# Kernel optimization log

Measured on AMD Instinct MI355X. Metric: run time of the kernel, lower is better.

## Reference

```python
import jax, jax.numpy as jnp
import numpy as np

B, L, D = 2, 2048, 2560
H, KV, HD = 8, 4, 256
FF = 10240
WINDOW = 1024
ROPE_BASE = 10000.0
EPS = 1e-6


def rmsnorm(x, scale=None):
    x32 = x.astype(jnp.float32)
    var = jnp.mean(jnp.square(x32), axis=-1, keepdims=True)
    xn = x32 * jax.lax.rsqrt(var + EPS)
    return xn if scale is None else xn * scale.astype(jnp.float32)


def apply_rope(x, positions, base):
    # full RoPE (rope_fraction=1.0): rotate pairs (i, i+head_dim//2)
    hd = x.shape[-1]
    half = hd // 2
    timescale = base ** (2.0 * jnp.arange(half, dtype=jnp.float32) / hd)
    ang = positions[:, :, None].astype(jnp.float32) / timescale  # [B,L,half]
    sin = jnp.sin(ang)[:, :, None, :]  # [B,L,1,half]
    cos = jnp.cos(ang)[:, :, None, :]
    x1, x2 = x[..., :half], x[..., half:]
    return jnp.concatenate([x1 * cos - x2 * sin, x2 * cos + x1 * sin], axis=-1)


def setup_inputs() -> dict:
    key = jax.random.key(0)
    ks = jax.random.split(key, 16)
    s = lambda fan_in: 1.0 / np.sqrt(fan_in)
    return {
        "x": jax.random.normal(ks[0], (B, L, D), jnp.float32),
        "positions": jnp.broadcast_to(jnp.arange(L, dtype=jnp.int32), (B, L)),
        "wq": jax.random.normal(ks[1], (D, H * HD), jnp.float32) * s(D),
        "wk": jax.random.normal(ks[2], (D, KV * HD), jnp.float32) * s(D),
        "wv": jax.random.normal(ks[3], (D, KV * HD), jnp.float32) * s(D),
        "wo": jax.random.normal(ks[4], (H * HD, D), jnp.float32) * s(H * HD),
        "q_scale": jnp.ones((HD,), jnp.float32),
        "k_scale": jnp.ones((HD,), jnp.float32),
        "pre_attn_scale": jnp.ones((D,), jnp.float32),
        "post_attn_scale": jnp.ones((D,), jnp.float32),
        "pre_ffw_scale": jnp.ones((D,), jnp.float32),
        "post_ffw_scale": jnp.ones((D,), jnp.float32),
        "w_gate": jax.random.normal(ks[5], (D, FF), jnp.float32) * s(D),
        "w_up": jax.random.normal(ks[6], (D, FF), jnp.float32) * s(D),
        "w_down": jax.random.normal(ks[7], (FF, D), jnp.float32) * s(FF),
    }


def reference(x, positions, wq, wk, wv, wo, q_scale, k_scale,
              pre_attn_scale, post_attn_scale, pre_ffw_scale, post_ffw_scale,
              w_gate, w_up, w_down):
    # --- attention sub-block ---
    h = rmsnorm(x, pre_attn_scale)
    q = (h @ wq).reshape(B, L, H, HD)
    k = (h @ wk).reshape(B, L, KV, HD)
    v = (h @ wv).reshape(B, L, KV, HD)
    q = apply_rope(rmsnorm(q, q_scale), positions, ROPE_BASE)
    k = apply_rope(rmsnorm(k, k_scale), positions, ROPE_BASE)
    v = rmsnorm(v)  # RMSNormNoScale on V
    rep = H // KV
    k = jnp.repeat(k, rep, axis=2)  # [B,L,H,HD]
    v = jnp.repeat(v, rep, axis=2)
    scores = jnp.einsum("bqhd,bkhd->bhqk", q, k)  # NOTE: no 1/sqrt(d) scaling, faithful to source
    i = jnp.arange(L)[:, None]
    j = jnp.arange(L)[None, :]
    mask = (j <= i) & (j > i - WINDOW)  # causal & sliding window
    scores = jnp.where(mask[None, None, :, :], scores, -10000.0)
    probs = jax.nn.softmax(scores.astype(jnp.float32), axis=-1)
    attn = jnp.einsum("bhqk,bkhd->bqhd", probs, v).reshape(B, L, H * HD)
    attn = attn @ wo
    x = x + rmsnorm(attn, post_attn_scale)
    # --- feedforward sub-block (GeGLU) ---
    h = rmsnorm(x, pre_ffw_scale)
    hidden = jax.nn.gelu(h @ w_gate, approximate=False) * (h @ w_up)
    ffw = hidden @ w_down
    x = x + rmsnorm(ffw, post_ffw_scale)
    return x
```

## Files before the change

### kernel.cpp

```cpp
#include <hip/hip_runtime.h>
#include <math.h>

#define DEV __device__ __forceinline__

typedef _Float16 f16;
typedef _Float16 f16x8 __attribute__((ext_vector_type(8)));
typedef _Float16 f16x4 __attribute__((ext_vector_type(4)));
typedef float f32x4 __attribute__((ext_vector_type(4)));

DEV void gload_lds16(const void* g, void* l) {
  __builtin_amdgcn_global_load_lds(
      (const __attribute__((address_space(1))) void*)g,
      (__attribute__((address_space(3))) void*)l, 16, 0, 0);
}

__global__ void transpose_w(const float* __restrict__ src, f16* __restrict__ dst,
                            int R, int C) {
  __shared__ float tile[32][33];
  int c0 = blockIdx.x * 32, r0 = blockIdx.y * 32;
  int tx = threadIdx.x, ty = threadIdx.y;
#pragma unroll
  for (int j = 0; j < 32; j += 8)
    tile[ty + j][tx] = src[(size_t)(r0 + ty + j) * C + c0 + tx];
  __syncthreads();
#pragma unroll
  for (int j = 0; j < 32; j += 8)
    dst[(size_t)(c0 + ty + j) * R + r0 + tx] = (f16)tile[tx][ty + j];
}

__global__ void rope_table_k(float* __restrict__ tab) {
  int idx = blockIdx.x * 256 + threadIdx.x;
  int pos = idx >> 7, j = idx & 127;
  float ts = powf(10000.0f, (float)j * (1.0f / 128.0f));
  float ang = (float)pos / ts;
  tab[pos * 256 + j] = sinf(ang);
  tab[pos * 256 + 128 + j] = cosf(ang);
}

__global__ __launch_bounds__(256) void rmsnorm_f32_f16(
    const float* __restrict__ in, const float* __restrict__ scale,
    f16* __restrict__ out) {
  constexpr int D = 2560, N4 = D / 4;
  const int m = blockIdx.x, tid = threadIdx.x;
  const float* row = in + (size_t)m * D;
  float vals[12];
  float ss = 0.f;
#pragma unroll
  for (int it = 0; it < 3; ++it) {
    int c4 = tid + it * 256;
    if (c4 < N4) {
      float4 v = *(const float4*)(row + c4 * 4);
      vals[it * 4 + 0] = v.x; vals[it * 4 + 1] = v.y;
      vals[it * 4 + 2] = v.z; vals[it * 4 + 3] = v.w;
      ss += v.x * v.x + v.y * v.y + v.z * v.z + v.w * v.w;
    }
  }
#pragma unroll
  for (int off = 32; off; off >>= 1) ss += __shfl_xor(ss, off, 64);
  __shared__ float red[4];
  if ((tid & 63) == 0) red[tid >> 6] = ss;
  __syncthreads();
  float rs = rsqrtf((red[0] + red[1] + red[2] + red[3]) * (1.0f / D) + 1e-6f);
#pragma unroll
  for (int it = 0; it < 3; ++it) {
    int c4 = tid + it * 256;
    if (c4 < N4) {
      float4 sc = *(const float4*)(scale + c4 * 4);
      f16x4 o;
      o[0] = (f16)(vals[it * 4 + 0] * rs * sc.x);
      o[1] = (f16)(vals[it * 4 + 1] * rs * sc.y);
      o[2] = (f16)(vals[it * 4 + 2] * rs * sc.z);
      o[3] = (f16)(vals[it * 4 + 3] * rs * sc.w);
      *(f16x4*)(out + (size_t)m * D + c4 * 4) = o;
    }
  }
}

__global__ __launch_bounds__(256) void residual_rmsnorm(
    const float* x, const f16* __restrict__ y,
    const float* __restrict__ scale, float* out) {
  constexpr int D = 2560, N4 = D / 4;
  const int m = blockIdx.x, tid = threadIdx.x;
  const f16* yr = y + (size_t)m * D;
  float yv[12];
  float ss = 0.f;
#pragma unroll
  for (int it = 0; it < 3; ++it) {
    int c4 = tid + it * 256;
    if (c4 < N4) {
      f16x4 u = *(const f16x4*)(yr + c4 * 4);
      float a = (float)u[0], b = (float)u[1], c = (float)u[2], d = (float)u[3];
      yv[it * 4 + 0] = a; yv[it * 4 + 1] = b; yv[it * 4 + 2] = c; yv[it * 4 + 3] = d;
      ss += a * a + b * b + c * c + d * d;
    }
  }
#pragma unroll
  for (int off = 32; off; off >>= 1) ss += __shfl_xor(ss, off, 64);
  __shared__ float red[4];
  if ((tid & 63) == 0) red[tid >> 6] = ss;
  __syncthreads();
  float rs = rsqrtf((red[0] + red[1] + red[2] + red[3]) * (1.0f / D) + 1e-6f);
#pragma unroll
  for (int it = 0; it < 3; ++it) {
    int c4 = tid + it * 256;
    if (c4 < N4) {
      float4 xv = *(const float4*)(x + (size_t)m * D + c4 * 4);
      float4 sc = *(const float4*)(scale + c4 * 4);
      float4 o;
      o.x = xv.x + yv[it * 4 + 0] * rs * sc.x;
      o.y = xv.y + yv[it * 4 + 1] * rs * sc.y;
      o.z = xv.z + yv[it * 4 + 2] * rs * sc.z;
      o.w = xv.w + yv[it * 4 + 3] * rs * sc.w;
      *(float4*)(out + (size_t)m * D + c4 * 4) = o;
    }
  }
}

__global__ __launch_bounds__(256) void norm_rope_k(
    const f16* __restrict__ qkv, const int* __restrict__ positions,
    const float* __restrict__ q_scale, const float* __restrict__ k_scale,
    const float* __restrict__ tab,
    f16* __restrict__ q_g, f16* __restrict__ k_g, f16* __restrict__ v_n) {
  const int m = blockIdx.x;
  const int tid = threadIdx.x, w = tid >> 6, l = tid & 63;
  const int pos = positions[m];
  const float* srow = tab + (size_t)pos * 256;
  const int c0 = l * 4;
  for (int vi = w; vi < 16; vi += 4) {
    f16x4 u = *(const f16x4*)(qkv + (size_t)m * 4096 + vi * 256 + c0);
    float x0 = (float)u[0], x1 = (float)u[1], x2 = (float)u[2], x3 = (float)u[3];
    float ss = x0 * x0 + x1 * x1 + x2 * x2 + x3 * x3;
#pragma unroll
    for (int off = 32; off; off >>= 1) ss += __shfl_xor(ss, off, 64);
    float rs = rsqrtf(ss * (1.0f / 256.0f) + 1e-6f);
    if (vi < 12) {
      const float* sc = (vi < 8) ? q_scale : k_scale;
      float4 s4 = *(const float4*)(sc + c0);
      float n0 = x0 * rs * s4.x, n1 = x1 * rs * s4.y;
      float n2 = x2 * rs * s4.z, n3 = x3 * rs * s4.w;
      float p0 = __shfl_xor(n0, 32, 64), p1 = __shfl_xor(n1, 32, 64);
      float p2 = __shfl_xor(n2, 32, 64), p3 = __shfl_xor(n3, 32, 64);
      int j0 = c0 & 127;
      float4 sn = *(const float4*)(srow + j0);
      float4 cs = *(const float4*)(srow + 128 + j0);
      float sgn = (l < 32) ? -1.0f : 1.0f;
      f16x4 o;
      o[0] = (f16)(n0 * cs.x + sgn * p0 * sn.x);
      o[1] = (f16)(n1 * cs.y + sgn * p1 * sn.y);
      o[2] = (f16)(n2 * cs.z + sgn * p2 * sn.z);
      o[3] = (f16)(n3 * cs.w + sgn * p3 * sn.w);
      if (vi < 8) *(f16x4*)(q_g + (size_t)m * 2048 + vi * 256 + c0) = o;
      else        *(f16x4*)(k_g + (size_t)m * 1024 + (vi - 8) * 256 + c0) = o;
    } else {
      f16x4 o;
      o[0] = (f16)(x0 * rs); o[1] = (f16)(x1 * rs);
      o[2] = (f16)(x2 * rs); o[3] = (f16)(x3 * rs);
      *(f16x4*)(v_n + (size_t)m * 1024 + (vi - 12) * 256 + c0) = o;
    }
  }
}

__global__ void transpose_v_k(const f16* __restrict__ v_n, f16* __restrict__ vt) {
  __shared__ f16 tile[32][33];
  int bkv = blockIdx.z;
  int b = bkv >> 2, kv = bkv & 3;
  int t0 = blockIdx.x * 32, d0 = blockIdx.y * 32;
  int tx = threadIdx.x, ty = threadIdx.y;
#pragma unroll
  for (int j = 0; j < 32; j += 8)
    tile[ty + j][tx] =
        v_n[(size_t)(b * 2048 + t0 + ty + j) * 1024 + kv * 256 + d0 + tx];
  __syncthreads();
#pragma unroll
  for (int j = 0; j < 32; j += 8)
    vt[((size_t)bkv * 256 + d0 + ty + j) * 2048 + t0 + tx] = tile[tx][ty + j];
}

template <int EPI>
__global__ __launch_bounds__(512, 2) void gemm256(
    const f16* __restrict__ A, const f16* __restrict__ BT,
    f16* __restrict__ C, const f16* __restrict__ aux, int M, int N, int K) {
  extern __shared__ __align__(16) f16 lds[];
  const int tid = threadIdx.x;
  const int w = tid >> 6, l = tid & 63;
  const int l15 = l & 15, lk = l >> 4;
  const int wm = w >> 2, wn = w & 3;

  const int orig = blockIdx.y * gridDim.x + blockIdx.x;
  const int bm = orig & 15;
  const int bn = orig >> 4;

  const int NT = K >> 6;

  const int srow = tid >> 2;
  const int sg = (tid & 3) ^ ((srow >> 1) & 3);
  const f16* pA1 = A + (size_t)(bm * 256 + srow) * K + sg * 8;
  const f16* pA2 = pA1 + (size_t)128 * K;
  const f16* pB1;
  const f16* pB2;
  if constexpr (EPI == 3) {
    pB1 = BT + (size_t)(bn * 128 + srow) * K + sg * 8;
    pB2 = aux + (size_t)(bn * 128 + srow) * K + sg * 8;
  } else {
    pB1 = BT + (size_t)(bn * 256 + srow) * K + sg * 8;
    pB2 = pB1 + (size_t)128 * K;
  }

  auto stage = [&](int op, int kh, int buf, int kt) {
    const int kb = kt * 64 + kh * 32;
    const f16* s1 = (op ? pB1 : pA1) + kb;
    const f16* s2 = (op ? pB2 : pA2) + kb;
    f16* dst = lds + ((buf << 2) + (kh << 1) + op) * 8192 + tid * 8;
    gload_lds16(s1, dst);
    gload_lds16(s2, dst + 4096);
  };

  const int fcol = (lk ^ ((l15 >> 1) & 3)) << 3;
  const int aoff = (wm * 128 + l15) * 32 + fcol;
  const int boff = 8192 + (wn * 64 + l15) * 32 + fcol;

  f32x4 acc[8][4] = {};

  stage(0, 0, 0, 0);
  stage(1, 0, 0, 0);
  stage(0, 1, 0, 0);
  stage(1, 1, 0, 0);
  if (NT > 1) stage(0, 0, 1, 1);
  asm volatile("s_waitcnt vmcnt(6)" ::: "memory");
  __builtin_amdgcn_s_barrier();
  asm volatile("" ::: "memory");

  for (int t = 0; t < NT; ++t) {
    const int buf = t & 1, nbuf = buf ^ 1;
    const f16* lb0 = lds + buf * 32768;
    const f16* lb1 = lb0 + 16384;
    {
      f16x8 a1[4], b[4], a2[4];
#pragma unroll
      for (int i = 0; i < 4; ++i) a1[i] = *(const f16x8*)(lb0 + aoff + i * 512);
#pragma unroll
      for (int i = 0; i < 4; ++i) b[i] = *(const f16x8*)(lb0 + boff + i * 512);
#pragma unroll
      for (int i = 0; i < 4; ++i) a2[i] = *(const f16x8*)(lb0 + aoff + (4 + i) * 512);
      if (t + 1 < NT) stage(1, 0, nbuf, t + 1);
      __builtin_amdgcn_s_setprio(1);
#pragma unroll
      for (int mi = 0; mi < 4; ++mi)
#pragma unroll
        for (int ni = 0; ni < 4; ++ni)
          acc[mi][ni] = __builtin_amdgcn_mfma_f32_16x16x32_f16(a1[mi], b[ni], acc[mi][ni], 0, 0, 0);
      __builtin_amdgcn_s_setprio(0);
      if (t + 1 < NT) stage(0, 1, nbuf, t + 1);
      __builtin_amdgcn_s_setprio(1);
#pragma unroll
      for (int mi = 0; mi < 4; ++mi)
#pragma unroll
        for (int ni = 0; ni < 4; ++ni)
          acc[4 + mi][ni] = __builtin_amdgcn_mfma_f32_16x16x32_f16(a2[mi], b[ni], acc[4 + mi][ni], 0, 0, 0);
      __builtin_amdgcn_s_setprio(0);
    }
    if (t + 1 < NT) asm volatile("s_waitcnt vmcnt(6)" ::: "memory");
    else            asm volatile("s_waitcnt vmcnt(0)" ::: "memory");
    __builtin_amdgcn_s_barrier();
    asm volatile("" ::: "memory");
    {
      f16x8 a1[4], b[4], a2[4];
#pragma unroll
      for (int i = 0; i < 4; ++i) a1[i] = *(const f16x8*)(lb1 + aoff + i * 512);
#pragma unroll
      for (int i = 0; i < 4; ++i) b[i] = *(const f16x8*)(lb1 + boff + i * 512);
#pragma unroll
      for (int i = 0; i < 4; ++i) a2[i] = *(const f16x8*)(lb1 + aoff + (4 + i) * 512);
      if (t + 1 < NT) stage(1, 1, nbuf, t + 1);
      __builtin_amdgcn_s_setprio(1);
#pragma unroll
      for (int mi = 0; mi < 4; ++mi)
#pragma unroll
        for (int ni = 0; ni < 4; ++ni)
          acc[mi][ni] = __builtin_amdgcn_mfma_f32_16x16x32_f16(a1[mi], b[ni], acc[mi][ni], 0, 0, 0);
      __builtin_amdgcn_s_setprio(0);
      if (t + 2 < NT) stage(0, 0, buf, t + 2);
      __builtin_amdgcn_s_setprio(1);
#pragma unroll
      for (int mi = 0; mi < 4; ++mi)
#pragma unroll
        for (int ni = 0; ni < 4; ++ni)
          acc[4 + mi][ni] = __builtin_amdgcn_mfma_f32_16x16x32_f16(a2[mi], b[ni], acc[4 + mi][ni], 0, 0, 0);
      __builtin_amdgcn_s_setprio(0);
    }
    if (t + 2 < NT)      asm volatile("s_waitcnt vmcnt(6)" ::: "memory");
    else if (t + 1 < NT) asm volatile("s_waitcnt vmcnt(4)" ::: "memory");
    else                 asm volatile("s_waitcnt vmcnt(0)" ::: "memory");
    __builtin_amdgcn_s_barrier();
    asm volatile("" ::: "memory");
  }

  if constexpr (EPI == 3) {
    constexpr int XP = 136;
    __syncthreads();
    f16* xls = lds;
    if (wn < 2) {
#pragma unroll
      for (int mi = 0; mi < 8; ++mi)
#pragma unroll
        for (int ni = 0; ni < 4; ++ni)
#pragma unroll
          for (int i = 0; i < 4; ++i) {
            int row = wm * 128 + mi * 16 + lk * 4 + i;
            int col = wn * 64 + ni * 16 + l15;
            float v = acc[mi][ni][i];
            v = 0.5f * v * (1.0f + erff(v * 0.70710678118654752f));
            xls[row * XP + col] = (f16)v;
          }
    }
    __syncthreads();
    if (wn >= 2) {
#pragma unroll
      for (int mi = 0; mi < 8; ++mi)
#pragma unroll
        for (int ni = 0; ni < 4; ++ni)
#pragma unroll
          for (int i = 0; i < 4; ++i) {
            int row = wm * 128 + mi * 16 + lk * 4 + i;
            int colg = (wn - 2) * 64 + ni * 16 + l15;
            float g = (float)xls[row * XP + colg];
            float v = g * acc[mi][ni][i];
            C[(size_t)(bm * 256 + row) * N + bn * 128 + colg] = (f16)v;
          }
    }
  } else {
#pragma unroll
    for (int mi = 0; mi < 8; ++mi) {
#pragma unroll
      for (int ni = 0; ni < 4; ++ni) {
#pragma unroll
        for (int i = 0; i < 4; ++i) {
          int row = bm * 256 + wm * 128 + mi * 16 + lk * 4 + i;
          int col = bn * 256 + wn * 64 + ni * 16 + l15;
          size_t idx = (size_t)row * N + col;
          float v = acc[mi][ni][i];
          if constexpr (EPI == 1) {
            v = 0.5f * v * (1.0f + erff(v * 0.70710678118654752f));
          } else if constexpr (EPI == 2) {
            v *= (float)aux[idx];
          }
          C[idx] = (f16)v;
        }
      }
    }
  }
}

__global__ __launch_bounds__(256) void flash_attn_k(
    const f16* __restrict__ q_g, const f16* __restrict__ k_g,
    const f16* __restrict__ vt, f16* __restrict__ ctx) {
  constexpr int KP = 264, VP = 40, PP = 40;
  __shared__ f16 Ks[32 * KP];
  __shared__ f16 Vs[256 * VP];
  __shared__ f16 Ps[4][16 * PP];
  const int qt = blockIdx.x, h = blockIdx.y, b = blockIdx.z;
  const int tid = threadIdx.x, w = tid >> 6, l = tid & 63;
  const int l15 = l & 15, lk = l >> 4;
  const int kv = h >> 1;

  f16x8 aq[8];
  const int qrow = qt * 64 + w * 16 + l15;
  const f16* qp = q_g + (size_t)(b * 2048 + qrow) * 2048 + h * 256 + lk * 8;
#pragma unroll
  for (int kc = 0; kc < 8; ++kc) aq[kc] = *(const f16x8*)(qp + kc * 32);

  f32x4 o[16] = {};
  float mrow[4] = {-1e30f, -1e30f, -1e30f, -1e30f};
  float lrow[4] = {0.f, 0.f, 0.f, 0.f};

  int kt_lo = 2 * qt - 32; if (kt_lo < 0) kt_lo = 0;
  const int kt_hi = 2 * qt + 1;
  const int iqb = qt * 64 + w * 16 + lk * 4;

  for (int kt = kt_lo; kt <= kt_hi; ++kt) {
    __syncthreads();
#pragma unroll
    for (int it = 0; it < 4; ++it) {
      int ch = tid + it * 256;
      int jl = ch >> 5, kcc = (ch & 31) * 8;
      *(f16x8*)&Ks[jl * KP + kcc] = *(const f16x8*)(
          k_g + (size_t)(b * 2048 + kt * 32 + jl) * 1024 + kv * 256 + kcc);
      int d = ch >> 2, tc = (ch & 3) * 8;
      *(f16x8*)&Vs[d * VP + tc] = *(const f16x8*)(
          vt + ((size_t)(b * 4 + kv) * 256 + d) * 2048 + kt * 32 + tc);
    }
    __syncthreads();
    f32x4 s[2] = {};
#pragma unroll
    for (int ct = 0; ct < 2; ++ct)
#pragma unroll
      for (int kc = 0; kc < 8; ++kc) {
        f16x8 bk = *(const f16x8*)&Ks[(ct * 16 + l15) * KP + kc * 32 + lk * 8];
        s[ct] = __builtin_amdgcn_mfma_f32_16x16x32_f16(aq[kc], bk, s[ct], 0, 0, 0);
      }
    float pm[4] = {-1e30f, -1e30f, -1e30f, -1e30f};
#pragma unroll
    for (int ct = 0; ct < 2; ++ct)
#pragma unroll
      for (int i = 0; i < 4; ++i) {
        int iq = iqb + i;
        int j = kt * 32 + ct * 16 + l15;
        bool valid = (j <= iq) && (j > iq - 1024);
        float sv = valid ? s[ct][i] : -1e30f;
        s[ct][i] = sv;
        pm[i] = fmaxf(pm[i], sv);
      }
#pragma unroll
    for (int i = 0; i < 4; ++i)
#pragma unroll
      for (int off = 1; off < 16; off <<= 1)
        pm[i] = fmaxf(pm[i], __shfl_xor(pm[i], off, 64));
    float corr[4], rsum[4];
#pragma unroll
    for (int i = 0; i < 4; ++i) {
      float mn = fmaxf(mrow[i], pm[i]);
      corr[i] = __expf(mrow[i] - mn);
      mrow[i] = mn;
      rsum[i] = 0.f;
    }
#pragma unroll
    for (int ct = 0; ct < 2; ++ct)
#pragma unroll
      for (int i = 0; i < 4; ++i) {
        float p = (s[ct][i] > -1e29f) ? __expf(s[ct][i] - mrow[i]) : 0.f;
        s[ct][i] = p;
        rsum[i] += p;
      }
#pragma unroll
    for (int i = 0; i < 4; ++i) {
#pragma unroll
      for (int off = 1; off < 16; off <<= 1) rsum[i] += __shfl_xor(rsum[i], off, 64);
      lrow[i] = lrow[i] * corr[i] + rsum[i];
    }
#pragma unroll
    for (int dt = 0; dt < 16; ++dt)
#pragma unroll
      for (int i = 0; i < 4; ++i) o[dt][i] *= corr[i];
#pragma unroll
    for (int ct = 0; ct < 2; ++ct)
#pragma unroll
      for (int i = 0; i < 4; ++i)
        Ps[w][(lk * 4 + i) * PP + ct * 16 + l15] = (f16)s[ct][i];
    __syncthreads();
    f16x8 pa = *(const f16x8*)&Ps[w][l15 * PP + lk * 8];
#pragma unroll
    for (int dt = 0; dt < 16; ++dt) {
      f16x8 bv = *(const f16x8*)&Vs[(dt * 16 + l15) * VP + lk * 8];
      o[dt] = __builtin_amdgcn_mfma_f32_16x16x32_f16(pa, bv, o[dt], 0, 0, 0);
    }
  }
  float inv[4];
#pragma unroll
  for (int i = 0; i < 4; ++i) inv[i] = 1.0f / lrow[i];
  f16* op = ctx + (size_t)(b * 2048 + qt * 64 + w * 16 + lk * 4) * 2048 + h * 256 + l15;
#pragma unroll
  for (int dt = 0; dt < 16; ++dt)
#pragma unroll
    for (int i = 0; i < 4; ++i)
      op[(size_t)i * 2048 + dt * 16] = (f16)(o[dt][i] * inv[i]);
}

extern "C" void kernel_launch(void* const* d_in, const int* in_sizes, int n_in,
                              void* d_out, int out_size, void* d_ws, size_t ws_size,
                              hipStream_t stream) {
  const float* x = (const float*)d_in[0];
  const int* positions = (const int*)d_in[1];
  const float* wq = (const float*)d_in[2];
  const float* wk = (const float*)d_in[3];
  const float* wv = (const float*)d_in[4];
  const float* wo = (const float*)d_in[5];
  const float* q_scale = (const float*)d_in[6];
  const float* k_scale = (const float*)d_in[7];
  const float* pre_attn = (const float*)d_in[8];
  const float* post_attn = (const float*)d_in[9];
  const float* pre_ffw = (const float*)d_in[10];
  const float* post_ffw = (const float*)d_in[11];
  const float* w_gate = (const float*)d_in[12];
  const float* w_up = (const float*)d_in[13];
  const float* w_down = (const float*)d_in[14];
  float* out = (float*)d_out;

  static bool s_attr = []() {
    hipFuncSetAttribute(reinterpret_cast<const void*>(&gemm256<0>),
                        hipFuncAttributeMaxDynamicSharedMemorySize, 131072);
    hipFuncSetAttribute(reinterpret_cast<const void*>(&gemm256<1>),
                        hipFuncAttributeMaxDynamicSharedMemorySize, 131072);
    hipFuncSetAttribute(reinterpret_cast<const void*>(&gemm256<2>),
                        hipFuncAttributeMaxDynamicSharedMemorySize, 131072);
    hipFuncSetAttribute(reinterpret_cast<const void*>(&gemm256<3>),
                        hipFuncAttributeMaxDynamicSharedMemorySize, 131072);
    return true;
  }();
  (void)s_attr;

  const size_t WT_BIG   = (size_t)20480 * 2560 * 2;
  const size_t WT_SMALL = (size_t)10240 * 2560 * 2;
  const size_t TAB_B = (size_t)2048 * 256 * 4;
  const size_t H_B   = (size_t)4096 * 2560 * 2;
  const size_t ACT_B = (size_t)92280832;
  auto aln = [](size_t v) { return (v + 255) & ~(size_t)255; };
  const bool big = ws_size >= aln(WT_BIG) + aln(TAB_B) + aln(H_B) + aln(ACT_B);

  char* ws = (char*)d_ws;
  size_t off = 0;
  auto alloc = [&](size_t bytes) {
    char* p = ws + off;
    off += (bytes + 255) & ~(size_t)255;
    return p;
  };
  f16* wT    = (f16*)alloc(big ? WT_BIG : WT_SMALL);
  float* tab = (float*)alloc(TAB_B);
  f16* h     = (f16*)alloc(H_B);
  char* act  = alloc(ACT_B);
  f16* qkv    = (f16*)(act);
  f16* q_g    = (f16*)(act + (size_t)33554432);
  f16* k_g    = (f16*)(act + (size_t)33554432 + 16777216);
  f16* v_n    = (f16*)(act + (size_t)33554432 + 16777216 + 8388608);
  f16* vtb    = (f16*)(act + (size_t)33554432 + 16777216 + 2 * 8388608);
  f16* ctx    = (f16*)(act + (size_t)33554432 + 16777216 + 3 * 8388608);
  f16* attn_o = (f16*)(act);
  f16* gbuf = (f16*)(act);
  f16* ffw  = h;
  f16* wuT  = wT + (size_t)10240 * 2560;
  (void)in_sizes; (void)n_in; (void)out_size;

  dim3 tb(32, 8);
  rope_table_k<<<1024, 256, 0, stream>>>(tab);

  rmsnorm_f32_f16<<<4096, 256, 0, stream>>>(x, pre_attn, h);
  transpose_w<<<dim3(2048 / 32, 2560 / 32), tb, 0, stream>>>(wq, wT, 2560, 2048);
  transpose_w<<<dim3(1024 / 32, 2560 / 32), tb, 0, stream>>>(wk, wT + (size_t)2048 * 2560, 2560, 1024);
  transpose_w<<<dim3(1024 / 32, 2560 / 32), tb, 0, stream>>>(wv, wT + (size_t)3072 * 2560, 2560, 1024);
  gemm256<0><<<dim3(4096 / 256, 4096 / 256), 512, 131072, stream>>>(h, wT, qkv, nullptr, 4096, 4096, 2560);
  norm_rope_k<<<4096, 256, 0, stream>>>(qkv, positions, q_scale, k_scale, tab, q_g, k_g, v_n);
  transpose_v_k<<<dim3(2048 / 32, 256 / 32, 8), tb, 0, stream>>>(v_n, vtb);
  flash_attn_k<<<dim3(32, 8, 2), 256, 0, stream>>>(q_g, k_g, vtb, ctx);
  transpose_w<<<dim3(2560 / 32, 2048 / 32), tb, 0, stream>>>(wo, wT, 2048, 2560);
  gemm256<0><<<dim3(2560 / 256, 4096 / 256), 512, 131072, stream>>>(ctx, wT, attn_o, nullptr, 4096, 2560, 2048);
  residual_rmsnorm<<<4096, 256, 0, stream>>>(x, attn_o, post_attn, out);

  rmsnorm_f32_f16<<<4096, 256, 0, stream>>>(out, pre_ffw, h);
  if (big) {
    transpose_w<<<dim3(10240 / 32, 2560 / 32), tb, 0, stream>>>(w_gate, wT, 2560, 10240);
    transpose_w<<<dim3(10240 / 32, 2560 / 32), tb, 0, stream>>>(w_up, wuT, 2560, 10240);
    gemm256<3><<<dim3(80, 16), 512, 131072, stream>>>(h, wT, gbuf, wuT, 4096, 10240, 2560);
  } else {
    transpose_w<<<dim3(10240 / 32, 2560 / 32), tb, 0, stream>>>(w_gate, wT, 2560, 10240);
    gemm256<1><<<dim3(10240 / 256, 4096 / 256), 512, 131072, stream>>>(h, wT, gbuf, nullptr, 4096, 10240, 2560);
    transpose_w<<<dim3(10240 / 32, 2560 / 32), tb, 0, stream>>>(w_up, wT, 2560, 10240);
    gemm256<2><<<dim3(10240 / 256, 4096 / 256), 512, 131072, stream>>>(h, wT, gbuf, gbuf, 4096, 10240, 2560);
  }
  transpose_w<<<dim3(2560 / 32, 10240 / 32), tb, 0, stream>>>(w_down, wT, 10240, 2560);
  gemm256<0><<<dim3(2560 / 256, 4096 / 256), 512, 131072, stream>>>(gbuf, wT, ffw, nullptr, 4096, 2560, 10240);
  residual_rmsnorm<<<4096, 256, 0, stream>>>(out, ffw, post_ffw, out);
}
```

Measured before the change: 1.196 ms.

## Add split-K for N=2560 GEMMs, vectorize weight transpose, fuse residual with pre-FFW norm

The output-projection and down-projection GEMMs (N=2560) launched only 160 tiles, so they now split K three ways into 480 blocks. The two extra partials are written as fp16 to workspace and summed inside the residual RMSNorm kernel. The weight transpose kernel moves to 64x64 tiles with float4 loads and 16-byte f16 stores. The post-attention residual is also fused with the pre-FFW RMSNorm, removing one kernel and one pass over the activations. In exchange, the partials add extra fp16 rounding and extra global traffic.

```diff
diff --git a/kernel.cpp b/kernel.cpp
--- a/kernel.cpp
+++ b/kernel.cpp
@@ -14,18 +14,31 @@
       (__attribute__((address_space(3))) void*)l, 16, 0, 0);
 }
 
-__global__ void transpose_w(const float* __restrict__ src, f16* __restrict__ dst,
-                            int R, int C) {
-  __shared__ float tile[32][33];
-  int c0 = blockIdx.x * 32, r0 = blockIdx.y * 32;
-  int tx = threadIdx.x, ty = threadIdx.y;
-#pragma unroll
-  for (int j = 0; j < 32; j += 8)
-    tile[ty + j][tx] = src[(size_t)(r0 + ty + j) * C + c0 + tx];
+__global__ __launch_bounds__(256) void transpose_w64(
+    const float* __restrict__ src, f16* __restrict__ dst, int R, int C) {
+  __shared__ float tile[64][65];
+  const int r0 = blockIdx.y * 64, c0 = blockIdx.x * 64;
+  const int tid = threadIdx.x;
+  const int rr = tid >> 4;
+  const int rc = (tid & 15) * 4;
+#pragma unroll
+  for (int p = 0; p < 4; ++p) {
+    int r = p * 16 + rr;
+    float4 v = *(const float4*)(src + (size_t)(r0 + r) * C + c0 + rc);
+    tile[r][rc] = v.x; tile[r][rc + 1] = v.y;
+    tile[r][rc + 2] = v.z; tile[r][rc + 3] = v.w;
+  }
   __syncthreads();
-#pragma unroll
-  for (int j = 0; j < 32; j += 8)
-    dst[(size_t)(c0 + ty + j) * R + r0 + tx] = (f16)tile[tx][ty + j];
+  const int wc = tid >> 3;
+  const int wk = (tid & 7) * 8;
+#pragma unroll
+  for (int p = 0; p < 2; ++p) {
+    int c = p * 32 + wc;
+    f16x8 o;
+#pragma unroll
+    for (int i = 0; i < 8; ++i) o[i] = (f16)tile[wk + i][c];
+    *(f16x8*)(dst + (size_t)(c0 + c) * R + r0 + wk) = o;
+  }
 }
 
 __global__ void rope_table_k(float* __restrict__ tab) {
@@ -76,42 +89,75 @@
   }
 }
 
-__global__ __launch_bounds__(256) void residual_rmsnorm(
-    const float* x, const f16* __restrict__ y,
-    const float* __restrict__ scale, float* out) {
+__global__ __launch_bounds__(256) void residual_rmsnorm3(
+    const float* __restrict__ x, const f16* __restrict__ y0,
+    const f16* __restrict__ y1, const f16* __restrict__ y2,
+    const float* __restrict__ scale, float* __restrict__ out,
+    const float* __restrict__ scale2, f16* __restrict__ h) {
   constexpr int D = 2560, N4 = D / 4;
   const int m = blockIdx.x, tid = threadIdx.x;
-  const f16* yr = y + (size_t)m * D;
+  const size_t base = (size_t)m * D;
+  __shared__ float red[4];
   float yv[12];
   float ss = 0.f;
 #pragma unroll
   for (int it = 0; it < 3; ++it) {
     int c4 = tid + it * 256;
     if (c4 < N4) {
-      f16x4 u = *(const f16x4*)(yr + c4 * 4);
+      f16x4 u = *(const f16x4*)(y0 + base + c4 * 4);
       float a = (float)u[0], b = (float)u[1], c = (float)u[2], d = (float)u[3];
+      if (y1) {
+        f16x4 v = *(const f16x4*)(y1 + base + c4 * 4);
+        f16x4 w2 = *(const f16x4*)(y2 + base + c4 * 4);
+        a += (float)v[0] + (float)w2[0]; b += (float)v[1] + (float)w2[1];
+        c += (float)v[2] + (float)w2[2]; d += (float)v[3] + (float)w2[3];
+      }
       yv[it * 4 + 0] = a; yv[it * 4 + 1] = b; yv[it * 4 + 2] = c; yv[it * 4 + 3] = d;
       ss += a * a + b * b + c * c + d * d;
     }
   }
 #pragma unroll
   for (int off = 32; off; off >>= 1) ss += __shfl_xor(ss, off, 64);
-  __shared__ float red[4];
   if ((tid & 63) == 0) red[tid >> 6] = ss;
   __syncthreads();
   float rs = rsqrtf((red[0] + red[1] + red[2] + red[3]) * (1.0f / D) + 1e-6f);
+  float ss2 = 0.f;
 #pragma unroll
   for (int it = 0; it < 3; ++it) {
     int c4 = tid + it * 256;
     if (c4 < N4) {
-      float4 xv = *(const float4*)(x + (size_t)m * D + c4 * 4);
+      float4 xv = *(const float4*)(x + base + c4 * 4);
       float4 sc = *(const float4*)(scale + c4 * 4);
       float4 o;
       o.x = xv.x + yv[it * 4 + 0] * rs * sc.x;
       o.y = xv.y + yv[it * 4 + 1] * rs * sc.y;
       o.z = xv.z + yv[it * 4 + 2] * rs * sc.z;
       o.w = xv.w + yv[it * 4 + 3] * rs * sc.w;
-      *(float4*)(out + (size_t)m * D + c4 * 4) = o;
+      *(float4*)(out + base + c4 * 4) = o;
+      yv[it * 4 + 0] = o.x; yv[it * 4 + 1] = o.y;
+      yv[it * 4 + 2] = o.z; yv[it * 4 + 3] = o.w;
+      ss2 += o.x * o.x + o.y * o.y + o.z * o.z + o.w * o.w;
+    }
+  }
+  if (h) {
+#pragma unroll
+    for (int off = 32; off; off >>= 1) ss2 += __shfl_xor(ss2, off, 64);
+    __syncthreads();
+    if ((tid & 63) == 0) red[tid >> 6] = ss2;
+    __syncthreads();
+    float rs2 = rsqrtf((red[0] + red[1] + red[2] + red[3]) * (1.0f / D) + 1e-6f);
+#pragma unroll
+    for (int it = 0; it < 3; ++it) {
+      int c4 = tid + it * 256;
+      if (c4 < N4) {
+        float4 sc = *(const float4*)(scale2 + c4 * 4);
+        f16x4 o;
+        o[0] = (f16)(yv[it * 4 + 0] * rs2 * sc.x);
+        o[1] = (f16)(yv[it * 4 + 1] * rs2 * sc.y);
+        o[2] = (f16)(yv[it * 4 + 2] * rs2 * sc.z);
+        o[3] = (f16)(yv[it * 4 + 3] * rs2 * sc.w);
+        *(f16x4*)(h + base + c4 * 4) = o;
+      }
     }
   }
 }
@@ -179,7 +225,8 @@
 template <int EPI>
 __global__ __launch_bounds__(512, 2) void gemm256(
     const f16* __restrict__ A, const f16* __restrict__ BT,
-    f16* __restrict__ C, const f16* __restrict__ aux, int M, int N, int K) {
+    f16* __restrict__ C, f16* __restrict__ aux, int M, int N, int K,
+    int kt0, int ktn) {
   extern __shared__ __align__(16) f16 lds[];
   const int tid = threadIdx.x;
   const int w = tid >> 6, l = tid & 63;
@@ -188,21 +235,35 @@
 
   const int orig = blockIdx.y * gridDim.x + blockIdx.x;
   const int bm = orig & 15;
-  const int bn = orig >> 4;
-
-  const int NT = K >> 6;
+  int bn, sK = 0;
+  if constexpr (EPI == 4) {
+    const int nper = (((int)(gridDim.x * gridDim.y)) >> 4) / 3;
+    const int q = orig >> 4;
+    bn = q % nper; sK = q / nper;
+  } else {
+    bn = orig >> 4;
+  }
+  int kt0v, ktnv;
+  if constexpr (EPI == 4) {
+    const int qt = ktn / 3, r = ktn % 3;
+    ktnv = qt + (sK < r ? 1 : 0);
+    kt0v = sK * qt + (sK < r ? sK : r);
+  } else {
+    kt0v = kt0; ktnv = ktn;
+  }
+  const int NT = ktnv;
 
   const int srow = tid >> 2;
   const int sg = (tid & 3) ^ ((srow >> 1) & 3);
-  const f16* pA1 = A + (size_t)(bm * 256 + srow) * K + sg * 8;
+  const f16* pA1 = A + (size_t)(bm * 256 + srow) * K + sg * 8 + kt0v * 64;
   const f16* pA2 = pA1 + (size_t)128 * K;
   const f16* pB1;
   const f16* pB2;
   if constexpr (EPI == 3) {
-    pB1 = BT + (size_t)(bn * 128 + srow) * K + sg * 8;
-    pB2 = aux + (size_t)(bn * 128 + srow) * K + sg * 8;
+    pB1 = BT + (size_t)(bn * 128 + srow) * K + sg * 8 + kt0v * 64;
+    pB2 = aux + (size_t)(bn * 128 + srow) * K + sg * 8 + kt0v * 64;
   } else {
-    pB1 = BT + (size_t)(bn * 256 + srow) * K + sg * 8;
+    pB1 = BT + (size_t)(bn * 256 + srow) * K + sg * 8 + kt0v * 64;
     pB2 = pB1 + (size_t)128 * K;
   }
 
@@ -329,6 +390,10 @@
           }
     }
   } else {
+    f16* Co = C;
+    if constexpr (EPI == 4) {
+      if (sK) Co = aux + (size_t)(sK - 1) * ((size_t)M * N);
+    }
 #pragma unroll
     for (int mi = 0; mi < 8; ++mi) {
 #pragma unroll
@@ -344,7 +409,7 @@
           } else if constexpr (EPI == 2) {
             v *= (float)aux[idx];
           }
-          C[idx] = (f16)v;
+          Co[idx] = (f16)v;
         }
       }
     }
@@ -493,6 +558,8 @@
     hipFuncSetAttribute(reinterpret_cast<const void*>(&gemm256<2>),
                         hipFuncAttributeMaxDynamicSharedMemorySize, 131072);
     hipFuncSetAttribute(reinterpret_cast<const void*>(&gemm256<3>),
+                        hipFuncAttributeMaxDynamicSharedMemorySize, 131072);
+    hipFuncSetAttribute(reinterpret_cast<const void*>(&gemm256<4>),
                         hipFuncAttributeMaxDynamicSharedMemorySize, 131072);
     return true;
   }();
@@ -527,35 +594,47 @@
   f16* gbuf = (f16*)(act);
   f16* ffw  = h;
   f16* wuT  = wT + (size_t)10240 * 2560;
+  f16* ap1  = wuT;
+  f16* fp1  = wT;
   (void)in_sizes; (void)n_in; (void)out_size;
 
-  dim3 tb(32, 8);
   rope_table_k<<<1024, 256, 0, stream>>>(tab);
 
   rmsnorm_f32_f16<<<4096, 256, 0, stream>>>(x, pre_attn, h);
-  transpose_w<<<dim3(2048 / 32, 2560 / 32), tb, 0, stream>>>(wq, wT, 2560, 2048);
-  transpose_w<<<dim3(1024 / 32, 2560 / 32), tb, 0, stream>>>(wk, wT + (size_t)2048 * 2560, 2560, 1024);
-  transpose_w<<<dim3(1024 / 32, 2560 / 32), tb, 0, stream>>>(wv, wT + (size_t)3072 * 2560, 2560, 1024);
-  gemm256<0><<<dim3(4096 / 256, 4096 / 256), 512, 131072, stream>>>(h, wT, qkv, nullptr, 4096, 4096, 2560);
+  transpose_w64<<<dim3(2048 / 64, 2560 / 64), 256, 0, stream>>>(wq, wT, 2560, 2048);
+  transpose_w64<<<dim3(1024 / 64, 2560 / 64), 256, 0, stream>>>(wk, wT + (size_t)2048 * 2560, 2560, 1024);
+  transpose_w64<<<dim3(1024 / 64, 2560 / 64), 256, 0, stream>>>(wv, wT + (size_t)3072 * 2560, 2560, 1024);
+  gemm256<0><<<dim3(16, 16), 512, 131072, stream>>>(h, wT, qkv, nullptr, 4096, 4096, 2560, 0, 40);
   norm_rope_k<<<4096, 256, 0, stream>>>(qkv, positions, q_scale, k_scale, tab, q_g, k_g, v_n);
-  transpose_v_k<<<dim3(2048 / 32, 256 / 32, 8), tb, 0, stream>>>(v_n, vtb);
+  transpose_v_k<<<dim3(2048 / 32, 256 / 32, 8), dim3(32, 8), 0, stream>>>(v_n, vtb);
   flash_attn_k<<<dim3(32, 8, 2), 256, 0, stream>>>(q_g, k_g, vtb, ctx);
-  transpose_w<<<dim3(2560 / 32, 2048 / 32), tb, 0, stream>>>(wo, wT, 2048, 2560);
-  gemm256<0><<<dim3(2560 / 256, 4096 / 256), 512, 131072, stream>>>(ctx, wT, attn_o, nullptr, 4096, 2560, 2048);
-  residual_rmsnorm<<<4096, 256, 0, stream>>>(x, attn_o, post_attn, out);
-
-  rmsnorm_f32_f16<<<4096, 256, 0, stream>>>(out, pre_ffw, h);
+  transpose_w64<<<dim3(2560 / 64, 2048 / 64), 256, 0, stream>>>(wo, wT, 2048, 2560);
   if (big) {
-    transpose_w<<<dim3(10240 / 32, 2560 / 32), tb, 0, stream>>>(w_gate, wT, 2560, 10240);
-    transpose_w<<<dim3(10240 / 32, 2560 / 32), tb, 0, stream>>>(w_up, wuT, 2560, 10240);
-    gemm256<3><<<dim3(80, 16), 512, 131072, stream>>>(h, wT, gbuf, wuT, 4096, 10240, 2560);
+    gemm256<4><<<dim3(30, 16), 512, 131072, stream>>>(ctx, wT, attn_o, ap1, 4096, 2560, 2048, 0, 32);
+    residual_rmsnorm3<<<4096, 256, 0, stream>>>(x, attn_o, ap1, ap1 + (size_t)4096 * 2560,
+                                                post_attn, out, pre_ffw, h);
   } else {
-    transpose_w<<<dim3(10240 / 32, 2560 / 32), tb, 0, stream>>>(w_gate, wT, 2560, 10240);
-    gemm256<1><<<dim3(10240 / 256, 4096 / 256), 512, 131072, stream>>>(h, wT, gbuf, nullptr, 4096, 10240, 2560);
-    transpose_w<<<dim3(10240 / 32, 2560 / 32), tb, 0, stream>>>(w_up, wT, 2560, 10240);
-    gemm256<2><<<dim3(10240 / 256, 4096 / 256), 512, 131072, stream>>>(h, wT, gbuf, gbuf, 4096, 10240, 2560);
-  }
-  transpose_w<<<dim3(2560 / 32, 10240 / 32), tb, 0, stream>>>(w_down, wT, 10240, 2560);
-  gemm256<0><<<dim3(2560 / 256, 4096 / 256), 512, 131072, stream>>>(gbuf, wT, ffw, nullptr, 4096, 2560, 10240);
-  residual_rmsnorm<<<4096, 256, 0, stream>>>(out, ffw, post_ffw, out);
-}
+    gemm256<0><<<dim3(10, 16), 512, 131072, stream>>>(ctx, wT, attn_o, nullptr, 4096, 2560, 2048, 0, 32);
+    residual_rmsnorm3<<<4096, 256, 0, stream>>>(x, attn_o, nullptr, nullptr,
+                                                post_attn, out, pre_ffw, h);
+  }
+
+  if (big) {
+    transpose_w64<<<dim3(10240 / 64, 2560 / 64), 256, 0, stream>>>(w_gate, wT, 2560, 10240);
+    transpose_w64<<<dim3(10240 / 64, 2560 / 64), 256, 0, stream>>>(w_up, wuT, 2560, 10240);
+    gemm256<3><<<dim3(80, 16), 512, 131072, stream>>>(h, wT, gbuf, wuT, 4096, 10240, 2560, 0, 40);
+    transpose_w64<<<dim3(2560 / 64, 10240 / 64), 256, 0, stream>>>(w_down, wuT, 10240, 2560);
+    gemm256<4><<<dim3(30, 16), 512, 131072, stream>>>(gbuf, wuT, ffw, fp1, 4096, 2560, 10240, 0, 160);
+    residual_rmsnorm3<<<4096, 256, 0, stream>>>(out, ffw, fp1, fp1 + (size_t)4096 * 2560,
+                                                post_ffw, out, nullptr, nullptr);
+  } else {
+    transpose_w64<<<dim3(10240 / 64, 2560 / 64), 256, 0, stream>>>(w_gate, wT, 2560, 10240);
+    gemm256<1><<<dim3(40, 16), 512, 131072, stream>>>(h, wT, gbuf, nullptr, 4096, 10240, 2560, 0, 40);
+    transpose_w64<<<dim3(10240 / 64, 2560 / 64), 256, 0, stream>>>(w_up, wT, 2560, 10240);
+    gemm256<2><<<dim3(40, 16), 512, 131072, stream>>>(h, wT, gbuf, gbuf, 4096, 10240, 2560, 0, 40);
+    transpose_w64<<<dim3(2560 / 64, 10240 / 64), 256, 0, stream>>>(w_down, wT, 10240, 2560);
+    gemm256<0><<<dim3(10, 16), 512, 131072, stream>>>(gbuf, wT, ffw, nullptr, 4096, 2560, 10240, 0, 160);
+    residual_rmsnorm3<<<4096, 256, 0, stream>>>(out, ffw, nullptr, nullptr,
+                                                post_ffw, out, nullptr, nullptr);
+  }
+}
```

Measured after the change: 1.154 ms. -3.5%, faster.
